# Kernel optimization log

Hardware: AMD Instinct MI355X
Metric: run time of the kernel (lower is better)

The kernel has to match this reference:

```python
import jax, jax.numpy as jnp
import numpy as np

B, NU, NT = 128, 32, 64          # batch, users/sample, antennas/sample
IN_F, H, OUT_F, NL = 128, 128, 16, 2
N_U, N_A = B * NU, B * NT        # total user / antenna nodes


def setup_inputs() -> dict:
    key = jax.random.key(0)
    ks = iter(jax.random.split(key, 40))
    p = lambda shape: jax.random.normal(next(ks), shape, jnp.float32) * 0.05
    inp = {
        'user_feat': jax.random.normal(next(ks), (N_U, IN_F), jnp.float32),
        'ant_noise': jax.random.normal(next(ks), (N_A, H), jnp.float32),
    }
    # complete bipartite edges within each batch sample
    b = np.arange(B)[:, None, None]
    u = np.arange(NU)[None, :, None]
    t = np.arange(NT)[None, None, :]
    su = np.broadcast_to(b * NU + u, (B, NU, NT)).reshape(-1)  # user global ids
    dt = np.broadcast_to(b * NT + t, (B, NU, NT)).reshape(-1)  # antenna global ids
    inp['src_u2a'] = jnp.asarray(su, jnp.int32)
    inp['dst_u2a'] = jnp.asarray(dt, jnp.int32)
    inp['src_a2u'] = jnp.asarray(dt, jnp.int32)
    inp['dst_a2u'] = jnp.asarray(su, jnp.int32)
    inp['W_ue'] = p((IN_F, H)); inp['b_ue'] = p((H,))
    inp['W_t'] = p((H, H));     inp['b_t'] = p((H,))
    for name in ['ca_aggr', 'ca_self', 'ca_comb', 'cu_aggr', 'cu_self', 'cu_comb']:
        inp[name + '_W'] = p((NL, H, H))
        inp[name + '_b'] = p((NL, H))
    inp['W_norm'] = p((H, OUT_F)); inp['b_norm'] = p((OUT_F,))
    return inp


def mlp(x, W, b):
    # stack of NL Linear(H,H) + ReLU, as in MLP module
    for i in range(W.shape[0]):
        x = jax.nn.relu(x @ W[i] + b[i])
    return x


def rel_conv(src_f, dst_f, src_idx, dst_idx, n_dst, aW, ab, sW, sb, cW, cb):
    # GraphConv2: mean-aggregate mlp_aggr(src) over in-edges, combine with mlp_self(dst)
    msg = mlp(src_f, aW, ab)                                   # [n_src, H]
    summed = jax.ops.segment_sum(msg[src_idx], dst_idx, num_segments=n_dst)
    deg = jax.ops.segment_sum(jnp.ones(dst_idx.shape, jnp.float32), dst_idx,
                              num_segments=n_dst)
    mean = summed / jnp.maximum(deg, 1.0)[:, None]
    return mlp(mlp(dst_f, sW, sb) + mean, cW, cb)


def reference(user_feat, ant_noise, src_u2a, dst_u2a, src_a2u, dst_a2u,
              W_ue, b_ue, W_t, b_t,
              ca_aggr_W, ca_aggr_b, ca_self_W, ca_self_b, ca_comb_W, ca_comb_b,
              cu_aggr_W, cu_aggr_b, cu_self_W, cu_self_b, cu_comb_W, cu_comb_b,
              W_norm, b_norm):
    # InitLayer
    hu = jax.nn.relu(user_feat @ W_ue + b_ue)                  # [B*NU, H]
    ant = jax.nn.relu(hu.reshape(B, NU, H).mean(axis=1) @ W_t + b_t)  # [B, H]
    ha = jnp.repeat(ant, NT, axis=0) + ant_noise               # [B*NT, H]
    # two applications of the SAME HeteroGraphConv (shared weights)
    for _ in range(2):
        na = rel_conv(hu, ha, src_u2a, dst_u2a, N_A,
                      ca_aggr_W, ca_aggr_b, ca_self_W, ca_self_b, ca_comb_W, ca_comb_b)
        nu = rel_conv(ha, hu, src_a2u, dst_a2u, N_U,
                      cu_aggr_W, cu_aggr_b, cu_self_W, cu_self_b, cu_comb_W, cu_comb_b)
        hu, ha = nu, na
    # NormLayer: project, split real/imag, normalize to unit modulus
    y = (ha @ W_norm + b_norm).reshape(B, NT, OUT_F)
    rf = OUT_F // 2
    re, im = y[..., :rf], y[..., rf:]
    mag = jnp.sqrt(re * re + im * im)
    return jnp.concatenate([re / mag, im / mag], axis=-1)      # [B, NT, OUT_F]
```

## Files before the change

### kernel.cpp

```cpp
#include <hip/hip_runtime.h>
#include <math.h>


using frag  = __attribute__((ext_vector_type(8))) short;
using f32x4 = __attribute__((ext_vector_type(4))) float;

#define LDST 136
#define SCOPE_AGT __HIP_MEMORY_SCOPE_AGENT

__device__ __forceinline__ float  bf2f(ushort u) { return __uint_as_float(((unsigned)u) << 16); }
__device__ __forceinline__ ushort f2bf(float f) {
    unsigned u = __float_as_uint(f);
    u += 0x7fff + ((u >> 16) & 1);
    return (ushort)(u >> 16);
}
__device__ __forceinline__ void gst4_sc(void* p, unsigned v) {
    asm volatile("global_store_dword %0, %1, off sc1" :: "v"(p), "v"(v) : "memory");
}

struct GP {
    const float *uf, *noise, *b_ue, *W_t, *b_t;
    const float *wsrc[13];
    const float *bias6[6];
    const float *Wn, *bn;
    float *out;
    ushort *WtAll;
    float *pE, *pA0, *pU0, *pA1;
    unsigned *cnt, *flg;
};

__device__ __forceinline__ void psync(unsigned* myf, unsigned* pf, unsigned s) {
    asm volatile("s_waitcnt vmcnt(0)" ::: "memory");
    __syncthreads();
    if (threadIdx.x == 0) {
        __hip_atomic_store(myf, s, __ATOMIC_RELAXED, SCOPE_AGT);
        while (__hip_atomic_load(pf, __ATOMIC_RELAXED, SCOPE_AGT) < s)
            __builtin_amdgcn_s_sleep(1);
    }
    __syncthreads();
}

template<int MT, bool MEANADD>
__device__ __forceinline__ void mlp_stage(const ushort* Xl, ushort* Yl,
    const ushort* __restrict__ Wt, const float* __restrict__ bias, const float* meanL)
{
    const int lane = threadIdx.x & 63, wave = threadIdx.x >> 6;
    const int q = lane >> 4, l15 = lane & 15;
    const int n0 = wave * 16;
    frag A[4];
#pragma unroll
    for (int kc = 0; kc < 4; ++kc)
        A[kc] = *(const frag*)(Wt + (n0 + l15) * 128 + kc * 32 + q * 8);
    const float4 bv = *(const float4*)(bias + n0 + q * 4);
    float4 mv = {0.f, 0.f, 0.f, 0.f};
    if (MEANADD) mv = *(const float4*)(meanL + n0 + q * 4);
#pragma unroll
    for (int mt = 0; mt < MT; ++mt) {
        frag Bv[4];
#pragma unroll
        for (int kc = 0; kc < 4; ++kc)
            Bv[kc] = *(const frag*)(Xl + (mt * 16 + l15) * LDST + kc * 32 + q * 8);
        f32x4 acc = {0.f, 0.f, 0.f, 0.f};
#pragma unroll
        for (int kc = 0; kc < 4; ++kc)
            acc = __builtin_amdgcn_mfma_f32_16x16x32_bf16(A[kc], Bv[kc], acc, 0, 0, 0);
        float v0 = acc[0] + bv.x, v1 = acc[1] + bv.y, v2 = acc[2] + bv.z, v3 = acc[3] + bv.w;
        v0 = v0 > 0.f ? v0 : 0.f; v1 = v1 > 0.f ? v1 : 0.f;
        v2 = v2 > 0.f ? v2 : 0.f; v3 = v3 > 0.f ? v3 : 0.f;
        if (MEANADD) { v0 += mv.x; v1 += mv.y; v2 += mv.z; v3 += mv.w; }
        ushort4 o = { f2bf(v0), f2bf(v1), f2bf(v2), f2bf(v3) };
        *(ushort4*)(Yl + (mt * 16 + l15) * LDST + n0 + q * 4) = o;
    }
}

template<int ROWS>
__device__ __forceinline__ void colsum(const ushort* buf, float* redL,
                                       float* ownDst, float* __restrict__ gDst)
{
    const int t = threadIdx.x, g = t >> 7, col = t & 127;
    float s = 0.f;
    for (int r = g; r < ROWS; r += 4) s += bf2f(buf[r * LDST + col]);
    redL[g * 128 + col] = s;
    __syncthreads();
    if (t < 128) {
        float tot = redL[t] + redL[128 + t] + redL[256 + t] + redL[384 + t];
        ownDst[t] = tot;
        gst4_sc(gDst + t, __float_as_uint(tot));
    }
    __syncthreads();
}

__device__ __forceinline__ void wslab(ushort* dst, float* slab,
                                      const float* __restrict__ W, int kb)
{
    {
        const int c = threadIdx.x;
        const int kr = c >> 5, c4 = c & 31;
        const float4 v = *(const float4*)(W + (kb * 16 + kr) * 128 + c4 * 4);
        slab[kr * 129 + c4 * 4 + 0] = v.x; slab[kr * 129 + c4 * 4 + 1] = v.y;
        slab[kr * 129 + c4 * 4 + 2] = v.z; slab[kr * 129 + c4 * 4 + 3] = v.w;
    }
    __syncthreads();
    for (int c = threadIdx.x; c < 1024; c += 512) {
        const int n = c >> 3, k2 = c & 7;
        const unsigned d = (unsigned)f2bf(slab[(2 * k2) * 129 + n])
                         | ((unsigned)f2bf(slab[(2 * k2 + 1) * 129 + n]) << 16);
        gst4_sc(dst + n * 128 + kb * 16 + 2 * k2, d);
    }
    __syncthreads();
}

__global__ __launch_bounds__(512, 1) void k_gnn(GP P)
{
    __shared__ __align__(16) ushort HU [16 * LDST];
    __shared__ __align__(16) ushort HU2[16 * LDST];
    __shared__ __align__(16) ushort HA [32 * LDST];
    __shared__ __align__(16) ushort HA2[32 * LDST];
    __shared__ __align__(16) ushort T0 [32 * LDST];
    __shared__ __align__(16) ushort T1 [32 * LDST];
    __shared__ float meanP[128], meanQ[128], antL[128], redL[512];

    const int blk = blockIdx.x, tid = threadIdx.x;
    const int b = blk >> 1, half = blk & 1;
    unsigned* myf = P.flg + blk * 32;
    unsigned* prf = P.flg + (blk ^ 1) * 32;
    const int prt = blk ^ 1;
    const ushort* Wt = P.WtAll;
    const float* const* bb = P.bias6;

    if (blk < 104)
        wslab(P.WtAll + (blk >> 3) * 16384, (float*)T1, P.wsrc[blk >> 3], blk & 7);

    {
        const int c = tid;
        const int r = c >> 5, k4 = c & 31;
        const float4 v = *(const float4*)(P.uf + (size_t)(b * 32 + half * 16 + r) * 128 + k4 * 4);
        ushort4 o = { f2bf(v.x), f2bf(v.y), f2bf(v.z), f2bf(v.w) };
        *(ushort4*)(T0 + r * LDST + k4 * 4) = o;
    }
    for (int c = tid; c < 1024; c += 512) {
        const int r = c >> 5, k4 = c & 31;
        const float4 v = *(const float4*)(P.noise + (size_t)(b * 64 + half * 32 + r) * 128 + k4 * 4);
        ushort4 o = { f2bf(v.x), f2bf(v.y), f2bf(v.z), f2bf(v.w) };
        *(ushort4*)(HA + r * LDST + k4 * 4) = o;
    }

    asm volatile("s_waitcnt vmcnt(0)" ::: "memory");
    __syncthreads();
    if (tid == 0) {
        if (blk < 104) {
            unsigned old = __hip_atomic_fetch_add(P.cnt, 1u, __ATOMIC_RELAXED, SCOPE_AGT);
            if (old == 103u) __hip_atomic_store(P.cnt + 32, 1u, __ATOMIC_RELAXED, SCOPE_AGT);
        }
        while (__hip_atomic_load(P.cnt + 32, __ATOMIC_RELAXED, SCOPE_AGT) < 1u)
            __builtin_amdgcn_s_sleep(4);
    }
    __syncthreads();

    mlp_stage<1, false>(T0, HU, Wt + 12 * 16384, P.b_ue, nullptr);
    __syncthreads();
    colsum<16>(HU, redL, meanP, P.pE + blk * 128);
    mlp_stage<1, false>(HU, T0, Wt + 0 * 16384, bb[0], nullptr);
    __syncthreads();
    mlp_stage<1, false>(T0, T1, Wt + 1 * 16384, bb[0] + 128, nullptr);
    __syncthreads();
    colsum<16>(T1, redL, meanQ, P.pA0 + blk * 128);
    psync(myf, prf, 1u);

    if (tid < 128) meanP[tid] = (meanP[tid] + P.pE[prt * 128 + tid]) * (1.f / 32.f);
    __syncthreads();
    {
        const int g = tid >> 7, col = tid & 127;
        float s = 0.f;
#pragma unroll 4
        for (int k = g * 32; k < g * 32 + 32; ++k) s += meanP[k] * P.W_t[k * 128 + col];
        redL[g * 128 + col] = s;
    }
    __syncthreads();
    if (tid < 128) {
        float a = P.b_t[tid] + redL[tid] + redL[128 + tid] + redL[256 + tid] + redL[384 + tid];
        antL[tid] = a > 0.f ? a : 0.f;
    }
    __syncthreads();
    for (int c = tid; c < 1024; c += 512) {
        const int r = c >> 5, k4 = c & 31;
        ushort4 h = *(ushort4*)(HA + r * LDST + k4 * 4);
        ushort4 o = { f2bf(bf2f(h.x) + antL[k4 * 4 + 0]), f2bf(bf2f(h.y) + antL[k4 * 4 + 1]),
                      f2bf(bf2f(h.z) + antL[k4 * 4 + 2]), f2bf(bf2f(h.w) + antL[k4 * 4 + 3]) };
        *(ushort4*)(HA + r * LDST + k4 * 4) = o;
    }
    __syncthreads();

    mlp_stage<2, false>(HA, T0, Wt + 6 * 16384, bb[3], nullptr);
    __syncthreads();
    mlp_stage<2, false>(T0, T1, Wt + 7 * 16384, bb[3] + 128, nullptr);
    __syncthreads();
    colsum<32>(T1, redL, meanP, P.pU0 + blk * 128);
    mlp_stage<2, false>(HA, T0, Wt + 2 * 16384, bb[1], nullptr);
    __syncthreads();
    psync(myf, prf, 2u);

    if (tid < 128) {
        meanQ[tid] = (meanQ[tid] + P.pA0[prt * 128 + tid]) * (1.f / 32.f);
        meanP[tid] = (meanP[tid] + P.pU0[prt * 128 + tid]) * (1.f / 64.f);
    }
    __syncthreads();
    mlp_stage<2, true >(T0, T1, Wt + 3 * 16384, bb[1] + 128, meanQ);
    __syncthreads();
    mlp_stage<2, false>(T1, T0, Wt + 4 * 16384, bb[2], nullptr);
    __syncthreads();
    mlp_stage<2, false>(T0, HA2, Wt + 5 * 16384, bb[2] + 128, nullptr);
    __syncthreads();
    mlp_stage<1, false>(HU, T0, Wt + 8 * 16384, bb[4], nullptr);
    __syncthreads();
    mlp_stage<1, true >(T0, T1, Wt + 9 * 16384, bb[4] + 128, meanP);
    __syncthreads();
    mlp_stage<1, false>(T1, T0, Wt + 10 * 16384, bb[5], nullptr);
    __syncthreads();
    mlp_stage<1, false>(T0, HU2, Wt + 11 * 16384, bb[5] + 128, nullptr);
    __syncthreads();

    mlp_stage<1, false>(HU2, T0, Wt + 0 * 16384, bb[0], nullptr);
    __syncthreads();
    mlp_stage<1, false>(T0, T1, Wt + 1 * 16384, bb[0] + 128, nullptr);
    __syncthreads();
    colsum<16>(T1, redL, meanQ, P.pA1 + blk * 128);
    mlp_stage<2, false>(HA2, T0, Wt + 2 * 16384, bb[1], nullptr);
    __syncthreads();
    psync(myf, prf, 3u);

    if (tid < 128) meanQ[tid] = (meanQ[tid] + P.pA1[prt * 128 + tid]) * (1.f / 32.f);
    __syncthreads();
    mlp_stage<2, true >(T0, T1, Wt + 3 * 16384, bb[1] + 128, meanQ);
    __syncthreads();
    mlp_stage<2, false>(T1, T0, Wt + 4 * 16384, bb[2], nullptr);
    __syncthreads();
    mlp_stage<2, false>(T0, T1, Wt + 5 * 16384, bb[2] + 128, nullptr);
    __syncthreads();

    float* WnS = (float*)T0;
    {
        const int c = tid;
        *(float4*)(WnS + c * 4) = *(const float4*)(P.Wn + c * 4);
    }
    __syncthreads();
    {
        const int row = tid >> 4, j = tid & 15;
        float acc = P.bn[j];
        const ushort* h = T1 + row * LDST;
#pragma unroll 4
        for (int k = 0; k < 128; ++k) acc += bf2f(h[k]) * WnS[k * 16 + j];
        redL[row * 16 + j] = acc;
        __syncthreads();
        const float re = redL[row * 16 + (j & 7)], im = redL[row * 16 + (j & 7) + 8];
        const float mag = sqrtf(re * re + im * im);
        const int a = b * 64 + half * 32 + row;
        P.out[a * 16 + j] = acc / mag;
    }
}

extern "C" void kernel_launch(void* const* d_in, const int* in_sizes, int n_in,
                              void* d_out, int out_size, void* d_ws, size_t ws_size,
                              hipStream_t stream)
{
    GP P;
    P.uf    = (const float*)d_in[0];
    P.noise = (const float*)d_in[1];
    const float* W_ue = (const float*)d_in[6];
    P.b_ue  = (const float*)d_in[7];
    P.W_t   = (const float*)d_in[8];
    P.b_t   = (const float*)d_in[9];
    const float* caW[3] = {(const float*)d_in[10], (const float*)d_in[12], (const float*)d_in[14]};
    const float* cab[3] = {(const float*)d_in[11], (const float*)d_in[13], (const float*)d_in[15]};
    const float* cuW[3] = {(const float*)d_in[16], (const float*)d_in[18], (const float*)d_in[20]};
    const float* cub[3] = {(const float*)d_in[17], (const float*)d_in[19], (const float*)d_in[21]};
    P.Wn  = (const float*)d_in[22];
    P.bn  = (const float*)d_in[23];
    P.out = (float*)d_out;

    P.wsrc[0]  = caW[0]; P.wsrc[1]  = caW[0] + 16384;
    P.wsrc[2]  = caW[1]; P.wsrc[3]  = caW[1] + 16384;
    P.wsrc[4]  = caW[2]; P.wsrc[5]  = caW[2] + 16384;
    P.wsrc[6]  = cuW[0]; P.wsrc[7]  = cuW[0] + 16384;
    P.wsrc[8]  = cuW[1]; P.wsrc[9]  = cuW[1] + 16384;
    P.wsrc[10] = cuW[2]; P.wsrc[11] = cuW[2] + 16384;
    P.wsrc[12] = W_ue;
    P.bias6[0] = cab[0]; P.bias6[1] = cab[1]; P.bias6[2] = cab[2];
    P.bias6[3] = cub[0]; P.bias6[4] = cub[1]; P.bias6[5] = cub[2];

    char* w = (char*)d_ws;
    P.cnt   = (unsigned*)w;
    P.flg   = (unsigned*)(w + 1024);
    P.WtAll = (ushort*)(w + 1024 + 32768);
    P.pE    = (float*)(P.WtAll + 13 * 16384);
    P.pA0   = P.pE  + 256 * 128;
    P.pU0   = P.pA0 + 256 * 128;
    P.pA1   = P.pU0 + 256 * 128;

    hipMemsetAsync(w, 0, 1024 + 32768, stream);
    k_gnn<<<dim3(256), dim3(512), 0, stream>>>(P);
}
```

Baseline: 140.3 us.

## Use one 1024-thread block per sample, removing pair sync and partial exchange

Each batch sample now runs in a single 1024-thread workgroup instead of two 512-thread workgroups. This removes the inter-block flag handshakes and the global partial-sum buffers used to share column means. Weight fragments for the next MLP stage are prefetched into registers during the current stage, and the final unit-modulus normalization uses a lane shuffle instead of a shared-memory round trip. In exchange, the grid drops from 256 to 128 blocks, so fewer compute units are busy, and each thread has more register pressure from the double-buffered fragments.

```diff
diff --git a/kernel.cpp b/kernel.cpp
--- a/kernel.cpp
+++ b/kernel.cpp
@@ -25,37 +25,28 @@
     const float *Wn, *bn;
     float *out;
     ushort *WtAll;
-    float *pE, *pA0, *pU0, *pA1;
-    unsigned *cnt, *flg;
+    unsigned *cnt;
 };
 
-__device__ __forceinline__ void psync(unsigned* myf, unsigned* pf, unsigned s) {
-    asm volatile("s_waitcnt vmcnt(0)" ::: "memory");
-    __syncthreads();
-    if (threadIdx.x == 0) {
-        __hip_atomic_store(myf, s, __ATOMIC_RELAXED, SCOPE_AGT);
-        while (__hip_atomic_load(pf, __ATOMIC_RELAXED, SCOPE_AGT) < s)
-            __builtin_amdgcn_s_sleep(1);
-    }
-    __syncthreads();
+struct AF { frag f[4]; };
+__device__ __forceinline__ AF loadA(const ushort* __restrict__ Wt, int n0, int l15, int q) {
+    AF r;
+#pragma unroll
+    for (int kc = 0; kc < 4; ++kc)
+        r.f[kc] = *(const frag*)(Wt + (n0 + l15) * 128 + kc * 32 + q * 8);
+    return r;
 }
 
 template<int MT, bool MEANADD>
-__device__ __forceinline__ void mlp_stage(const ushort* Xl, ushort* Yl,
-    const ushort* __restrict__ Wt, const float* __restrict__ bias, const float* meanL)
-{
-    const int lane = threadIdx.x & 63, wave = threadIdx.x >> 6;
-    const int q = lane >> 4, l15 = lane & 15;
-    const int n0 = wave * 16;
-    frag A[4];
-#pragma unroll
-    for (int kc = 0; kc < 4; ++kc)
-        A[kc] = *(const frag*)(Wt + (n0 + l15) * 128 + kc * 32 + q * 8);
+__device__ __forceinline__ void mlp_stage(const AF& A, const ushort* Xl, ushort* Yl,
+    const float* __restrict__ bias, const float* meanL, int n0, int l15, int q, int mg)
+{
     const float4 bv = *(const float4*)(bias + n0 + q * 4);
     float4 mv = {0.f, 0.f, 0.f, 0.f};
     if (MEANADD) mv = *(const float4*)(meanL + n0 + q * 4);
 #pragma unroll
-    for (int mt = 0; mt < MT; ++mt) {
+    for (int i = 0; i < MT / 2; ++i) {
+        const int mt = mg * (MT / 2) + i;
         frag Bv[4];
 #pragma unroll
         for (int kc = 0; kc < 4; ++kc)
@@ -63,7 +54,7 @@
         f32x4 acc = {0.f, 0.f, 0.f, 0.f};
 #pragma unroll
         for (int kc = 0; kc < 4; ++kc)
-            acc = __builtin_amdgcn_mfma_f32_16x16x32_bf16(A[kc], Bv[kc], acc, 0, 0, 0);
+            acc = __builtin_amdgcn_mfma_f32_16x16x32_bf16(A.f[kc], Bv[kc], acc, 0, 0, 0);
         float v0 = acc[0] + bv.x, v1 = acc[1] + bv.y, v2 = acc[2] + bv.z, v3 = acc[3] + bv.w;
         v0 = v0 > 0.f ? v0 : 0.f; v1 = v1 > 0.f ? v1 : 0.f;
         v2 = v2 > 0.f ? v2 : 0.f; v3 = v3 > 0.f ? v3 : 0.f;
@@ -74,26 +65,24 @@
 }
 
 template<int ROWS>
-__device__ __forceinline__ void colsum(const ushort* buf, float* redL,
-                                       float* ownDst, float* __restrict__ gDst)
-{
-    const int t = threadIdx.x, g = t >> 7, col = t & 127;
-    float s = 0.f;
-    for (int r = g; r < ROWS; r += 4) s += bf2f(buf[r * LDST + col]);
-    redL[g * 128 + col] = s;
-    __syncthreads();
-    if (t < 128) {
-        float tot = redL[t] + redL[128 + t] + redL[256 + t] + redL[384 + t];
-        ownDst[t] = tot;
-        gst4_sc(gDst + t, __float_as_uint(tot));
-    }
+__device__ __forceinline__ void colmean(const ushort* buf, float* redL, float* dst, float scale) {
+    const int t = threadIdx.x;
+    if (t < 512) {
+        const int g4 = t >> 7, col = t & 127;
+        float s = 0.f;
+#pragma unroll
+        for (int r = g4; r < ROWS; r += 4) s += bf2f(buf[r * LDST + col]);
+        redL[g4 * 128 + col] = s;
+    }
+    __syncthreads();
+    if (t < 128) dst[t] = (redL[t] + redL[128 + t] + redL[256 + t] + redL[384 + t]) * scale;
     __syncthreads();
 }
 
 __device__ __forceinline__ void wslab(ushort* dst, float* slab,
                                       const float* __restrict__ W, int kb)
 {
-    {
+    if (threadIdx.x < 512) {
         const int c = threadIdx.x;
         const int kr = c >> 5, c4 = c & 31;
         const float4 v = *(const float4*)(W + (kb * 16 + kr) * 128 + c4 * 4);
@@ -101,7 +90,8 @@
         slab[kr * 129 + c4 * 4 + 2] = v.z; slab[kr * 129 + c4 * 4 + 3] = v.w;
     }
     __syncthreads();
-    for (int c = threadIdx.x; c < 1024; c += 512) {
+    {
+        const int c = threadIdx.x;
         const int n = c >> 3, k2 = c & 7;
         const unsigned d = (unsigned)f2bf(slab[(2 * k2) * 129 + n])
                          | ((unsigned)f2bf(slab[(2 * k2 + 1) * 129 + n]) << 16);
@@ -110,37 +100,34 @@
     __syncthreads();
 }
 
-__global__ __launch_bounds__(512, 1) void k_gnn(GP P)
-{
-    __shared__ __align__(16) ushort HU [16 * LDST];
-    __shared__ __align__(16) ushort HU2[16 * LDST];
-    __shared__ __align__(16) ushort HA [32 * LDST];
-    __shared__ __align__(16) ushort HA2[32 * LDST];
-    __shared__ __align__(16) ushort T0 [32 * LDST];
-    __shared__ __align__(16) ushort T1 [32 * LDST];
-    __shared__ float meanP[128], meanQ[128], antL[128], redL[512];
-
-    const int blk = blockIdx.x, tid = threadIdx.x;
-    const int b = blk >> 1, half = blk & 1;
-    unsigned* myf = P.flg + blk * 32;
-    unsigned* prf = P.flg + (blk ^ 1) * 32;
-    const int prt = blk ^ 1;
+__global__ __launch_bounds__(1024, 1) void k_gnn(GP P)
+{
+    __shared__ __align__(16) ushort HU[32 * LDST];
+    __shared__ __align__(16) ushort HA[64 * LDST];
+    __shared__ __align__(16) ushort T0[64 * LDST];
+    __shared__ __align__(16) ushort T1[64 * LDST];
+    __shared__ float redL[512], mA[128], mB[128];
+
+    const int b = blockIdx.x, tid = threadIdx.x;
+    const int lane = tid & 63, wave = tid >> 6;
+    const int q = lane >> 4, l15 = lane & 15;
+    const int n0 = (wave & 7) * 16, mg = wave >> 3;
     const ushort* Wt = P.WtAll;
     const float* const* bb = P.bias6;
 
-    if (blk < 104)
-        wslab(P.WtAll + (blk >> 3) * 16384, (float*)T1, P.wsrc[blk >> 3], blk & 7);
+    if (b < 104)
+        wslab(P.WtAll + (b >> 3) * 16384, (float*)T1, P.wsrc[b >> 3], b & 7);
 
     {
-        const int c = tid;
-        const int r = c >> 5, k4 = c & 31;
-        const float4 v = *(const float4*)(P.uf + (size_t)(b * 32 + half * 16 + r) * 128 + k4 * 4);
+        const int r = tid >> 5, k4 = tid & 31;
+        const float4 v = *(const float4*)(P.uf + (size_t)(b * 32 + r) * 128 + k4 * 4);
         ushort4 o = { f2bf(v.x), f2bf(v.y), f2bf(v.z), f2bf(v.w) };
         *(ushort4*)(T0 + r * LDST + k4 * 4) = o;
     }
-    for (int c = tid; c < 1024; c += 512) {
+#pragma unroll
+    for (int c = tid; c < 2048; c += 1024) {
         const int r = c >> 5, k4 = c & 31;
-        const float4 v = *(const float4*)(P.noise + (size_t)(b * 64 + half * 32 + r) * 128 + k4 * 4);
+        const float4 v = *(const float4*)(P.noise + (size_t)(b * 64 + r) * 128 + k4 * 4);
         ushort4 o = { f2bf(v.x), f2bf(v.y), f2bf(v.z), f2bf(v.w) };
         *(ushort4*)(HA + r * LDST + k4 * 4) = o;
     }
@@ -148,7 +135,7 @@
     asm volatile("s_waitcnt vmcnt(0)" ::: "memory");
     __syncthreads();
     if (tid == 0) {
-        if (blk < 104) {
+        if (b < 104) {
             unsigned old = __hip_atomic_fetch_add(P.cnt, 1u, __ATOMIC_RELAXED, SCOPE_AGT);
             if (old == 103u) __hip_atomic_store(P.cnt + 32, 1u, __ATOMIC_RELAXED, SCOPE_AGT);
         }
@@ -157,105 +144,110 @@
     }
     __syncthreads();
 
-    mlp_stage<1, false>(T0, HU, Wt + 12 * 16384, P.b_ue, nullptr);
-    __syncthreads();
-    colsum<16>(HU, redL, meanP, P.pE + blk * 128);
-    mlp_stage<1, false>(HU, T0, Wt + 0 * 16384, bb[0], nullptr);
-    __syncthreads();
-    mlp_stage<1, false>(T0, T1, Wt + 1 * 16384, bb[0] + 128, nullptr);
-    __syncthreads();
-    colsum<16>(T1, redL, meanQ, P.pA0 + blk * 128);
-    psync(myf, prf, 1u);
-
-    if (tid < 128) meanP[tid] = (meanP[tid] + P.pE[prt * 128 + tid]) * (1.f / 32.f);
-    __syncthreads();
-    {
-        const int g = tid >> 7, col = tid & 127;
+    AF A, An = loadA(Wt + 12 * 16384, n0, l15, q);
+
+    A = An; An = loadA(Wt + 0 * 16384, n0, l15, q);
+    mlp_stage<2, false>(A, T0, HU, P.b_ue, nullptr, n0, l15, q, mg);
+    __syncthreads();
+    colmean<32>(HU, redL, mA, 1.f / 32.f);
+    if (tid < 512) {
+        const int g4 = tid >> 7, col = tid & 127;
         float s = 0.f;
 #pragma unroll 4
-        for (int k = g * 32; k < g * 32 + 32; ++k) s += meanP[k] * P.W_t[k * 128 + col];
-        redL[g * 128 + col] = s;
+        for (int k = g4 * 32; k < g4 * 32 + 32; ++k) s += mA[k] * P.W_t[k * 128 + col];
+        redL[g4 * 128 + col] = s;
     }
     __syncthreads();
     if (tid < 128) {
         float a = P.b_t[tid] + redL[tid] + redL[128 + tid] + redL[256 + tid] + redL[384 + tid];
-        antL[tid] = a > 0.f ? a : 0.f;
-    }
-    __syncthreads();
-    for (int c = tid; c < 1024; c += 512) {
+        mB[tid] = a > 0.f ? a : 0.f;
+    }
+    __syncthreads();
+#pragma unroll
+    for (int c = tid; c < 2048; c += 1024) {
         const int r = c >> 5, k4 = c & 31;
         ushort4 h = *(ushort4*)(HA + r * LDST + k4 * 4);
-        ushort4 o = { f2bf(bf2f(h.x) + antL[k4 * 4 + 0]), f2bf(bf2f(h.y) + antL[k4 * 4 + 1]),
-                      f2bf(bf2f(h.z) + antL[k4 * 4 + 2]), f2bf(bf2f(h.w) + antL[k4 * 4 + 3]) };
+        ushort4 o = { f2bf(bf2f(h.x) + mB[k4 * 4 + 0]), f2bf(bf2f(h.y) + mB[k4 * 4 + 1]),
+                      f2bf(bf2f(h.z) + mB[k4 * 4 + 2]), f2bf(bf2f(h.w) + mB[k4 * 4 + 3]) };
         *(ushort4*)(HA + r * LDST + k4 * 4) = o;
     }
     __syncthreads();
 
-    mlp_stage<2, false>(HA, T0, Wt + 6 * 16384, bb[3], nullptr);
-    __syncthreads();
-    mlp_stage<2, false>(T0, T1, Wt + 7 * 16384, bb[3] + 128, nullptr);
-    __syncthreads();
-    colsum<32>(T1, redL, meanP, P.pU0 + blk * 128);
-    mlp_stage<2, false>(HA, T0, Wt + 2 * 16384, bb[1], nullptr);
-    __syncthreads();
-    psync(myf, prf, 2u);
-
-    if (tid < 128) {
-        meanQ[tid] = (meanQ[tid] + P.pA0[prt * 128 + tid]) * (1.f / 32.f);
-        meanP[tid] = (meanP[tid] + P.pU0[prt * 128 + tid]) * (1.f / 64.f);
-    }
-    __syncthreads();
-    mlp_stage<2, true >(T0, T1, Wt + 3 * 16384, bb[1] + 128, meanQ);
-    __syncthreads();
-    mlp_stage<2, false>(T1, T0, Wt + 4 * 16384, bb[2], nullptr);
-    __syncthreads();
-    mlp_stage<2, false>(T0, HA2, Wt + 5 * 16384, bb[2] + 128, nullptr);
-    __syncthreads();
-    mlp_stage<1, false>(HU, T0, Wt + 8 * 16384, bb[4], nullptr);
-    __syncthreads();
-    mlp_stage<1, true >(T0, T1, Wt + 9 * 16384, bb[4] + 128, meanP);
-    __syncthreads();
-    mlp_stage<1, false>(T1, T0, Wt + 10 * 16384, bb[5], nullptr);
-    __syncthreads();
-    mlp_stage<1, false>(T0, HU2, Wt + 11 * 16384, bb[5] + 128, nullptr);
-    __syncthreads();
-
-    mlp_stage<1, false>(HU2, T0, Wt + 0 * 16384, bb[0], nullptr);
-    __syncthreads();
-    mlp_stage<1, false>(T0, T1, Wt + 1 * 16384, bb[0] + 128, nullptr);
-    __syncthreads();
-    colsum<16>(T1, redL, meanQ, P.pA1 + blk * 128);
-    mlp_stage<2, false>(HA2, T0, Wt + 2 * 16384, bb[1], nullptr);
-    __syncthreads();
-    psync(myf, prf, 3u);
-
-    if (tid < 128) meanQ[tid] = (meanQ[tid] + P.pA1[prt * 128 + tid]) * (1.f / 32.f);
-    __syncthreads();
-    mlp_stage<2, true >(T0, T1, Wt + 3 * 16384, bb[1] + 128, meanQ);
-    __syncthreads();
-    mlp_stage<2, false>(T1, T0, Wt + 4 * 16384, bb[2], nullptr);
-    __syncthreads();
-    mlp_stage<2, false>(T0, T1, Wt + 5 * 16384, bb[2] + 128, nullptr);
+    A = An; An = loadA(Wt + 1 * 16384, n0, l15, q);
+    mlp_stage<2, false>(A, HU, T0, bb[0], nullptr, n0, l15, q, mg);
+    __syncthreads();
+    A = An; An = loadA(Wt + 6 * 16384, n0, l15, q);
+    mlp_stage<2, false>(A, T0, T1, bb[0] + 128, nullptr, n0, l15, q, mg);
+    __syncthreads();
+    colmean<32>(T1, redL, mA, 1.f / 32.f);
+
+    A = An; An = loadA(Wt + 7 * 16384, n0, l15, q);
+    mlp_stage<4, false>(A, HA, T0, bb[3], nullptr, n0, l15, q, mg);
+    __syncthreads();
+    A = An; An = loadA(Wt + 2 * 16384, n0, l15, q);
+    mlp_stage<4, false>(A, T0, T1, bb[3] + 128, nullptr, n0, l15, q, mg);
+    __syncthreads();
+    colmean<64>(T1, redL, mB, 1.f / 64.f);
+
+    A = An; An = loadA(Wt + 3 * 16384, n0, l15, q);
+    mlp_stage<4, false>(A, HA, T0, bb[1], nullptr, n0, l15, q, mg);
+    __syncthreads();
+    A = An; An = loadA(Wt + 4 * 16384, n0, l15, q);
+    mlp_stage<4, true >(A, T0, T1, bb[1] + 128, mA, n0, l15, q, mg);
+    __syncthreads();
+    A = An; An = loadA(Wt + 5 * 16384, n0, l15, q);
+    mlp_stage<4, false>(A, T1, T0, bb[2], nullptr, n0, l15, q, mg);
+    __syncthreads();
+    A = An; An = loadA(Wt + 8 * 16384, n0, l15, q);
+    mlp_stage<4, false>(A, T0, HA, bb[2] + 128, nullptr, n0, l15, q, mg);
+    __syncthreads();
+
+    A = An; An = loadA(Wt + 9 * 16384, n0, l15, q);
+    mlp_stage<2, false>(A, HU, T0, bb[4], nullptr, n0, l15, q, mg);
+    __syncthreads();
+    A = An; An = loadA(Wt + 10 * 16384, n0, l15, q);
+    mlp_stage<2, true >(A, T0, T1, bb[4] + 128, mB, n0, l15, q, mg);
+    __syncthreads();
+    A = An; An = loadA(Wt + 11 * 16384, n0, l15, q);
+    mlp_stage<2, false>(A, T1, T0, bb[5], nullptr, n0, l15, q, mg);
+    __syncthreads();
+    A = An; An = loadA(Wt + 0 * 16384, n0, l15, q);
+    mlp_stage<2, false>(A, T0, HU, bb[5] + 128, nullptr, n0, l15, q, mg);
+    __syncthreads();
+
+    A = An; An = loadA(Wt + 1 * 16384, n0, l15, q);
+    mlp_stage<2, false>(A, HU, T0, bb[0], nullptr, n0, l15, q, mg);
+    __syncthreads();
+    A = An; An = loadA(Wt + 2 * 16384, n0, l15, q);
+    mlp_stage<2, false>(A, T0, T1, bb[0] + 128, nullptr, n0, l15, q, mg);
+    __syncthreads();
+    colmean<32>(T1, redL, mA, 1.f / 32.f);
+
+    A = An; An = loadA(Wt + 3 * 16384, n0, l15, q);
+    mlp_stage<4, false>(A, HA, T0, bb[1], nullptr, n0, l15, q, mg);
+    __syncthreads();
+    A = An; An = loadA(Wt + 4 * 16384, n0, l15, q);
+    mlp_stage<4, true >(A, T0, T1, bb[1] + 128, mA, n0, l15, q, mg);
+    __syncthreads();
+    A = An; An = loadA(Wt + 5 * 16384, n0, l15, q);
+    mlp_stage<4, false>(A, T1, T0, bb[2], nullptr, n0, l15, q, mg);
+    __syncthreads();
+    A = An;
+    mlp_stage<4, false>(A, T0, T1, bb[2] + 128, nullptr, n0, l15, q, mg);
     __syncthreads();
 
     float* WnS = (float*)T0;
-    {
-        const int c = tid;
-        *(float4*)(WnS + c * 4) = *(const float4*)(P.Wn + c * 4);
-    }
+    if (tid < 512) *(float4*)(WnS + tid * 4) = *(const float4*)(P.Wn + tid * 4);
     __syncthreads();
     {
         const int row = tid >> 4, j = tid & 15;
         float acc = P.bn[j];
         const ushort* h = T1 + row * LDST;
-#pragma unroll 4
+#pragma unroll 8
         for (int k = 0; k < 128; ++k) acc += bf2f(h[k]) * WnS[k * 16 + j];
-        redL[row * 16 + j] = acc;
-        __syncthreads();
-        const float re = redL[row * 16 + (j & 7)], im = redL[row * 16 + (j & 7) + 8];
-        const float mag = sqrtf(re * re + im * im);
-        const int a = b * 64 + half * 32 + row;
-        P.out[a * 16 + j] = acc / mag;
+        const float other = __shfl_xor(acc, 8);
+        const float mag = sqrtf(acc * acc + other * other);
+        P.out[(size_t)(b * 64 + row) * 16 + j] = acc / mag;
     }
 }
 
@@ -290,13 +282,8 @@
 
     char* w = (char*)d_ws;
     P.cnt   = (unsigned*)w;
-    P.flg   = (unsigned*)(w + 1024);
-    P.WtAll = (ushort*)(w + 1024 + 32768);
-    P.pE    = (float*)(P.WtAll + 13 * 16384);
-    P.pA0   = P.pE  + 256 * 128;
-    P.pU0   = P.pA0 + 256 * 128;
-    P.pA1   = P.pU0 + 256 * 128;
-
-    hipMemsetAsync(w, 0, 1024 + 32768, stream);
-    k_gnn<<<dim3(256), dim3(512), 0, stream>>>(P);
-}
+    P.WtAll = (ushort*)(w + 1024);
+
+    hipMemsetAsync(w, 0, 1024, stream);
+    k_gnn<<<dim3(128), dim3(1024), 0, stream>>>(P);
+}
```

New measurement: 149.2 us. +6.4%, slower.

## Drop global weight-transpose phase; prefetch fp32 weights per stage into registers

Applied to the files above, without the earlier changes.

Removes the initial phase where 104 blocks converted weights to a transposed bf16 workspace, along with the grid-wide barrier that made every block wait for it. Each wave now loads its fp32 weight slice straight from global memory, converts it to bf16 fragments in registers, and prefetches the next stage's weights while the current MFMA stage runs. Biases are staged once in LDS, one mean update is moved earlier, and the final normalisation uses a lane shuffle in place of an LDS round trip. The trade is that every block repeats strided, uncoalesced fp32 weight reads and conversion work, and the prefetch buffer adds about 32 registers per thread.

```diff
diff --git a/kernel.cpp b/kernel.cpp
--- a/kernel.cpp
+++ b/kernel.cpp
@@ -20,13 +20,12 @@
 
 struct GP {
     const float *uf, *noise, *b_ue, *W_t, *b_t;
-    const float *wsrc[13];
+    const float *Wm[13];
     const float *bias6[6];
     const float *Wn, *bn;
     float *out;
-    ushort *WtAll;
     float *pE, *pA0, *pU0, *pA1;
-    unsigned *cnt, *flg;
+    unsigned *flg;
 };
 
 __device__ __forceinline__ void psync(unsigned* myf, unsigned* pf, unsigned s) {
@@ -40,18 +39,35 @@
     __syncthreads();
 }
 
+struct PF { float v[32]; };
+struct AF { frag f[4]; };
+__device__ __forceinline__ PF prefA(const float* __restrict__ W, int n0, int l15, int q) {
+    PF p;
+    const float* base = W + (size_t)(q * 8) * 128 + n0 + l15;
+#pragma unroll
+    for (int kc = 0; kc < 4; ++kc)
+#pragma unroll
+        for (int j = 0; j < 8; ++j)
+            p.v[kc * 8 + j] = base[(kc * 32 + j) * 128];
+    return p;
+}
+__device__ __forceinline__ AF convA(const PF& p) {
+    AF a;
+#pragma unroll
+    for (int kc = 0; kc < 4; ++kc) {
+        frag f;
+#pragma unroll
+        for (int j = 0; j < 8; ++j) f[j] = (short)f2bf(p.v[kc * 8 + j]);
+        a.f[kc] = f;
+    }
+    return a;
+}
+
 template<int MT, bool MEANADD>
-__device__ __forceinline__ void mlp_stage(const ushort* Xl, ushort* Yl,
-    const ushort* __restrict__ Wt, const float* __restrict__ bias, const float* meanL)
+__device__ __forceinline__ void mlp_stage(const AF& A, const ushort* Xl, ushort* Yl,
+    const float* biasL, const float* meanL, int n0, int l15, int q)
 {
-    const int lane = threadIdx.x & 63, wave = threadIdx.x >> 6;
-    const int q = lane >> 4, l15 = lane & 15;
-    const int n0 = wave * 16;
-    frag A[4];
-#pragma unroll
-    for (int kc = 0; kc < 4; ++kc)
-        A[kc] = *(const frag*)(Wt + (n0 + l15) * 128 + kc * 32 + q * 8);
-    const float4 bv = *(const float4*)(bias + n0 + q * 4);
+    const float4 bv = *(const float4*)(biasL + n0 + q * 4);
     float4 mv = {0.f, 0.f, 0.f, 0.f};
     if (MEANADD) mv = *(const float4*)(meanL + n0 + q * 4);
 #pragma unroll
@@ -63,7 +79,7 @@
         f32x4 acc = {0.f, 0.f, 0.f, 0.f};
 #pragma unroll
         for (int kc = 0; kc < 4; ++kc)
-            acc = __builtin_amdgcn_mfma_f32_16x16x32_bf16(A[kc], Bv[kc], acc, 0, 0, 0);
+            acc = __builtin_amdgcn_mfma_f32_16x16x32_bf16(A.f[kc], Bv[kc], acc, 0, 0, 0);
         float v0 = acc[0] + bv.x, v1 = acc[1] + bv.y, v2 = acc[2] + bv.z, v3 = acc[3] + bv.w;
         v0 = v0 > 0.f ? v0 : 0.f; v1 = v1 > 0.f ? v1 : 0.f;
         v2 = v2 > 0.f ? v2 : 0.f; v3 = v3 > 0.f ? v3 : 0.f;
@@ -79,6 +95,7 @@
 {
     const int t = threadIdx.x, g = t >> 7, col = t & 127;
     float s = 0.f;
+#pragma unroll
     for (int r = g; r < ROWS; r += 4) s += bf2f(buf[r * LDST + col]);
     redL[g * 128 + col] = s;
     __syncthreads();
@@ -90,84 +107,64 @@
     __syncthreads();
 }
 
-__device__ __forceinline__ void wslab(ushort* dst, float* slab,
-                                      const float* __restrict__ W, int kb)
-{
-    {
-        const int c = threadIdx.x;
-        const int kr = c >> 5, c4 = c & 31;
-        const float4 v = *(const float4*)(W + (kb * 16 + kr) * 128 + c4 * 4);
-        slab[kr * 129 + c4 * 4 + 0] = v.x; slab[kr * 129 + c4 * 4 + 1] = v.y;
-        slab[kr * 129 + c4 * 4 + 2] = v.z; slab[kr * 129 + c4 * 4 + 3] = v.w;
-    }
-    __syncthreads();
-    for (int c = threadIdx.x; c < 1024; c += 512) {
-        const int n = c >> 3, k2 = c & 7;
-        const unsigned d = (unsigned)f2bf(slab[(2 * k2) * 129 + n])
-                         | ((unsigned)f2bf(slab[(2 * k2 + 1) * 129 + n]) << 16);
-        gst4_sc(dst + n * 128 + kb * 16 + 2 * k2, d);
-    }
-    __syncthreads();
-}
-
 __global__ __launch_bounds__(512, 1) void k_gnn(GP P)
 {
-    __shared__ __align__(16) ushort HU [16 * LDST];
-    __shared__ __align__(16) ushort HU2[16 * LDST];
-    __shared__ __align__(16) ushort HA [32 * LDST];
-    __shared__ __align__(16) ushort HA2[32 * LDST];
-    __shared__ __align__(16) ushort T0 [32 * LDST];
-    __shared__ __align__(16) ushort T1 [32 * LDST];
-    __shared__ float meanP[128], meanQ[128], antL[128], redL[512];
+    __shared__ __align__(16) ushort HU[16 * LDST];
+    __shared__ __align__(16) ushort HA[32 * LDST];
+    __shared__ __align__(16) ushort T0[32 * LDST];
+    __shared__ __align__(16) ushort T1[32 * LDST];
+    __shared__ __align__(16) float  biasL[1792];
+    __shared__ __align__(16) float  redL[512];
+    __shared__ __align__(16) float  meanP[128], meanQ[128], antL[128];
 
     const int blk = blockIdx.x, tid = threadIdx.x;
-    const int b = blk >> 1, half = blk & 1;
+    const int b = blk >> 1, half = blk & 1, prt = blk ^ 1;
+    const int lane = tid & 63, wave = tid >> 6;
+    const int q = lane >> 4, l15 = lane & 15;
+    const int n0 = wave * 16;
     unsigned* myf = P.flg + blk * 32;
-    unsigned* prf = P.flg + (blk ^ 1) * 32;
-    const int prt = blk ^ 1;
-    const ushort* Wt = P.WtAll;
-    const float* const* bb = P.bias6;
-
-    if (blk < 104)
-        wslab(P.WtAll + (blk >> 3) * 16384, (float*)T1, P.wsrc[blk >> 3], blk & 7);
+    unsigned* prf = P.flg + prt * 32;
+
+    PF p = prefA(P.Wm[12], n0, l15, q);
 
     {
-        const int c = tid;
-        const int r = c >> 5, k4 = c & 31;
+        const int r = tid >> 5, k4 = tid & 31;
         const float4 v = *(const float4*)(P.uf + (size_t)(b * 32 + half * 16 + r) * 128 + k4 * 4);
         ushort4 o = { f2bf(v.x), f2bf(v.y), f2bf(v.z), f2bf(v.w) };
         *(ushort4*)(T0 + r * LDST + k4 * 4) = o;
     }
+#pragma unroll
     for (int c = tid; c < 1024; c += 512) {
         const int r = c >> 5, k4 = c & 31;
         const float4 v = *(const float4*)(P.noise + (size_t)(b * 64 + half * 32 + r) * 128 + k4 * 4);
         ushort4 o = { f2bf(v.x), f2bf(v.y), f2bf(v.z), f2bf(v.w) };
         *(ushort4*)(HA + r * LDST + k4 * 4) = o;
     }
-
-    asm volatile("s_waitcnt vmcnt(0)" ::: "memory");
-    __syncthreads();
-    if (tid == 0) {
-        if (blk < 104) {
-            unsigned old = __hip_atomic_fetch_add(P.cnt, 1u, __ATOMIC_RELAXED, SCOPE_AGT);
-            if (old == 103u) __hip_atomic_store(P.cnt + 32, 1u, __ATOMIC_RELAXED, SCOPE_AGT);
-        }
-        while (__hip_atomic_load(P.cnt + 32, __ATOMIC_RELAXED, SCOPE_AGT) < 1u)
-            __builtin_amdgcn_s_sleep(4);
-    }
-    __syncthreads();
-
-    mlp_stage<1, false>(T0, HU, Wt + 12 * 16384, P.b_ue, nullptr);
+    if (tid < 128) biasL[tid] = P.b_ue[tid];
+    if (tid < 128) biasL[1664 + tid] = P.b_t[tid];
+#pragma unroll
+    for (int r = 0; r < 6; ++r)
+        if (tid < 256) biasL[128 + r * 256 + tid] = P.bias6[r][tid];
+    __syncthreads();
+
+    AF A;
+    A = convA(p); p = prefA(P.Wm[0], n0, l15, q);
+    mlp_stage<1, false>(A, T0, HU, biasL + 0, nullptr, n0, l15, q);
     __syncthreads();
     colsum<16>(HU, redL, meanP, P.pE + blk * 128);
-    mlp_stage<1, false>(HU, T0, Wt + 0 * 16384, bb[0], nullptr);
-    __syncthreads();
-    mlp_stage<1, false>(T0, T1, Wt + 1 * 16384, bb[0] + 128, nullptr);
+    A = convA(p); p = prefA(P.Wm[1], n0, l15, q);
+    mlp_stage<1, false>(A, HU, T0, biasL + 128, nullptr, n0, l15, q);
+    __syncthreads();
+    A = convA(p); p = prefA(P.Wm[6], n0, l15, q);
+    mlp_stage<1, false>(A, T0, T1, biasL + 256, nullptr, n0, l15, q);
     __syncthreads();
     colsum<16>(T1, redL, meanQ, P.pA0 + blk * 128);
     psync(myf, prf, 1u);
 
-    if (tid < 128) meanP[tid] = (meanP[tid] + P.pE[prt * 128 + tid]) * (1.f / 32.f);
+    if (tid < 128) {
+        meanP[tid] = (meanP[tid] + P.pE[prt * 128 + tid]) * (1.f / 32.f);
+        meanQ[tid] = (meanQ[tid] + P.pA0[prt * 128 + tid]) * (1.f / 32.f);
+    }
     __syncthreads();
     {
         const int g = tid >> 7, col = tid & 127;
@@ -178,10 +175,11 @@
     }
     __syncthreads();
     if (tid < 128) {
-        float a = P.b_t[tid] + redL[tid] + redL[128 + tid] + redL[256 + tid] + redL[384 + tid];
+        float a = biasL[1664 + tid] + redL[tid] + redL[128 + tid] + redL[256 + tid] + redL[384 + tid];
         antL[tid] = a > 0.f ? a : 0.f;
     }
     __syncthreads();
+#pragma unroll
     for (int c = tid; c < 1024; c += 512) {
         const int r = c >> 5, k4 = c & 31;
         ushort4 h = *(ushort4*)(HA + r * LDST + k4 * 4);
@@ -191,71 +189,78 @@
     }
     __syncthreads();
 
-    mlp_stage<2, false>(HA, T0, Wt + 6 * 16384, bb[3], nullptr);
-    __syncthreads();
-    mlp_stage<2, false>(T0, T1, Wt + 7 * 16384, bb[3] + 128, nullptr);
+    A = convA(p); p = prefA(P.Wm[7], n0, l15, q);
+    mlp_stage<2, false>(A, HA, T0, biasL + 896, nullptr, n0, l15, q);
+    __syncthreads();
+    A = convA(p); p = prefA(P.Wm[2], n0, l15, q);
+    mlp_stage<2, false>(A, T0, T1, biasL + 1024, nullptr, n0, l15, q);
     __syncthreads();
     colsum<32>(T1, redL, meanP, P.pU0 + blk * 128);
-    mlp_stage<2, false>(HA, T0, Wt + 2 * 16384, bb[1], nullptr);
+    A = convA(p); p = prefA(P.Wm[3], n0, l15, q);
+    mlp_stage<2, false>(A, HA, T0, biasL + 384, nullptr, n0, l15, q);
     __syncthreads();
     psync(myf, prf, 2u);
-
-    if (tid < 128) {
-        meanQ[tid] = (meanQ[tid] + P.pA0[prt * 128 + tid]) * (1.f / 32.f);
+    if (tid < 128)
         meanP[tid] = (meanP[tid] + P.pU0[prt * 128 + tid]) * (1.f / 64.f);
-    }
-    __syncthreads();
-    mlp_stage<2, true >(T0, T1, Wt + 3 * 16384, bb[1] + 128, meanQ);
-    __syncthreads();
-    mlp_stage<2, false>(T1, T0, Wt + 4 * 16384, bb[2], nullptr);
-    __syncthreads();
-    mlp_stage<2, false>(T0, HA2, Wt + 5 * 16384, bb[2] + 128, nullptr);
-    __syncthreads();
-    mlp_stage<1, false>(HU, T0, Wt + 8 * 16384, bb[4], nullptr);
-    __syncthreads();
-    mlp_stage<1, true >(T0, T1, Wt + 9 * 16384, bb[4] + 128, meanP);
-    __syncthreads();
-    mlp_stage<1, false>(T1, T0, Wt + 10 * 16384, bb[5], nullptr);
-    __syncthreads();
-    mlp_stage<1, false>(T0, HU2, Wt + 11 * 16384, bb[5] + 128, nullptr);
-    __syncthreads();
-
-    mlp_stage<1, false>(HU2, T0, Wt + 0 * 16384, bb[0], nullptr);
-    __syncthreads();
-    mlp_stage<1, false>(T0, T1, Wt + 1 * 16384, bb[0] + 128, nullptr);
+    __syncthreads();
+    A = convA(p); p = prefA(P.Wm[4], n0, l15, q);
+    mlp_stage<2, true >(A, T0, T1, biasL + 512, meanQ, n0, l15, q);
+    __syncthreads();
+    A = convA(p); p = prefA(P.Wm[5], n0, l15, q);
+    mlp_stage<2, false>(A, T1, T0, biasL + 640, nullptr, n0, l15, q);
+    __syncthreads();
+    A = convA(p); p = prefA(P.Wm[8], n0, l15, q);
+    mlp_stage<2, false>(A, T0, HA, biasL + 768, nullptr, n0, l15, q);
+    __syncthreads();
+    A = convA(p); p = prefA(P.Wm[9], n0, l15, q);
+    mlp_stage<1, false>(A, HU, T0, biasL + 1152, nullptr, n0, l15, q);
+    __syncthreads();
+    A = convA(p); p = prefA(P.Wm[10], n0, l15, q);
+    mlp_stage<1, true >(A, T0, T1, biasL + 1280, meanP, n0, l15, q);
+    __syncthreads();
+    A = convA(p); p = prefA(P.Wm[11], n0, l15, q);
+    mlp_stage<1, false>(A, T1, T0, biasL + 1408, nullptr, n0, l15, q);
+    __syncthreads();
+    A = convA(p); p = prefA(P.Wm[0], n0, l15, q);
+    mlp_stage<1, false>(A, T0, HU, biasL + 1536, nullptr, n0, l15, q);
+    __syncthreads();
+
+    A = convA(p); p = prefA(P.Wm[1], n0, l15, q);
+    mlp_stage<1, false>(A, HU, T0, biasL + 128, nullptr, n0, l15, q);
+    __syncthreads();
+    A = convA(p); p = prefA(P.Wm[2], n0, l15, q);
+    mlp_stage<1, false>(A, T0, T1, biasL + 256, nullptr, n0, l15, q);
     __syncthreads();
     colsum<16>(T1, redL, meanQ, P.pA1 + blk * 128);
-    mlp_stage<2, false>(HA2, T0, Wt + 2 * 16384, bb[1], nullptr);
+    A = convA(p); p = prefA(P.Wm[3], n0, l15, q);
+    mlp_stage<2, false>(A, HA, T0, biasL + 384, nullptr, n0, l15, q);
     __syncthreads();
     psync(myf, prf, 3u);
-
-    if (tid < 128) meanQ[tid] = (meanQ[tid] + P.pA1[prt * 128 + tid]) * (1.f / 32.f);
-    __syncthreads();
-    mlp_stage<2, true >(T0, T1, Wt + 3 * 16384, bb[1] + 128, meanQ);
-    __syncthreads();
-    mlp_stage<2, false>(T1, T0, Wt + 4 * 16384, bb[2], nullptr);
-    __syncthreads();
-    mlp_stage<2, false>(T0, T1, Wt + 5 * 16384, bb[2] + 128, nullptr);
+    if (tid < 128)
+        meanQ[tid] = (meanQ[tid] + P.pA1[prt * 128 + tid]) * (1.f / 32.f);
+    __syncthreads();
+    A = convA(p); p = prefA(P.Wm[4], n0, l15, q);
+    mlp_stage<2, true >(A, T0, T1, biasL + 512, meanQ, n0, l15, q);
+    __syncthreads();
+    A = convA(p); p = prefA(P.Wm[5], n0, l15, q);
+    mlp_stage<2, false>(A, T1, T0, biasL + 640, nullptr, n0, l15, q);
+    __syncthreads();
+    A = convA(p);
+    mlp_stage<2, false>(A, T0, T1, biasL + 768, nullptr, n0, l15, q);
     __syncthreads();
 
     float* WnS = (float*)T0;
-    {
-        const int c = tid;
-        *(float4*)(WnS + c * 4) = *(const float4*)(P.Wn + c * 4);
-    }
+    *(float4*)(WnS + tid * 4) = *(const float4*)(P.Wn + tid * 4);
     __syncthreads();
     {
         const int row = tid >> 4, j = tid & 15;
         float acc = P.bn[j];
         const ushort* h = T1 + row * LDST;
-#pragma unroll 4
+#pragma unroll 8
         for (int k = 0; k < 128; ++k) acc += bf2f(h[k]) * WnS[k * 16 + j];
-        redL[row * 16 + j] = acc;
-        __syncthreads();
-        const float re = redL[row * 16 + (j & 7)], im = redL[row * 16 + (j & 7) + 8];
-        const float mag = sqrtf(re * re + im * im);
-        const int a = b * 64 + half * 32 + row;
-        P.out[a * 16 + j] = acc / mag;
+        const float other = __shfl_xor(acc, 8);
+        const float mag = sqrtf(acc * acc + other * other);
+        P.out[(size_t)(b * 64 + half * 32 + row) * 16 + j] = acc / mag;
     }
 }
 
@@ -278,25 +283,23 @@
     P.bn  = (const float*)d_in[23];
     P.out = (float*)d_out;
 
-    P.wsrc[0]  = caW[0]; P.wsrc[1]  = caW[0] + 16384;
-    P.wsrc[2]  = caW[1]; P.wsrc[3]  = caW[1] + 16384;
-    P.wsrc[4]  = caW[2]; P.wsrc[5]  = caW[2] + 16384;
-    P.wsrc[6]  = cuW[0]; P.wsrc[7]  = cuW[0] + 16384;
-    P.wsrc[8]  = cuW[1]; P.wsrc[9]  = cuW[1] + 16384;
-    P.wsrc[10] = cuW[2]; P.wsrc[11] = cuW[2] + 16384;
-    P.wsrc[12] = W_ue;
+    P.Wm[0]  = caW[0]; P.Wm[1]  = caW[0] + 16384;
+    P.Wm[2]  = caW[1]; P.Wm[3]  = caW[1] + 16384;
+    P.Wm[4]  = caW[2]; P.Wm[5]  = caW[2] + 16384;
+    P.Wm[6]  = cuW[0]; P.Wm[7]  = cuW[0] + 16384;
+    P.Wm[8]  = cuW[1]; P.Wm[9]  = cuW[1] + 16384;
+    P.Wm[10] = cuW[2]; P.Wm[11] = cuW[2] + 16384;
+    P.Wm[12] = W_ue;
     P.bias6[0] = cab[0]; P.bias6[1] = cab[1]; P.bias6[2] = cab[2];
     P.bias6[3] = cub[0]; P.bias6[4] = cub[1]; P.bias6[5] = cub[2];
 
     char* w = (char*)d_ws;
-    P.cnt   = (unsigned*)w;
-    P.flg   = (unsigned*)(w + 1024);
-    P.WtAll = (ushort*)(w + 1024 + 32768);
-    P.pE    = (float*)(P.WtAll + 13 * 16384);
-    P.pA0   = P.pE  + 256 * 128;
-    P.pU0   = P.pA0 + 256 * 128;
-    P.pA1   = P.pU0 + 256 * 128;
-
-    hipMemsetAsync(w, 0, 1024 + 32768, stream);
+    P.flg = (unsigned*)w;
+    P.pE  = (float*)(w + 32768);
+    P.pA0 = P.pE  + 256 * 128;
+    P.pU0 = P.pA0 + 256 * 128;
+    P.pA1 = P.pU0 + 256 * 128;
+
+    hipMemsetAsync(w, 0, 32768, stream);
     k_gnn<<<dim3(256), dim3(512), 0, stream>>>(P);
 }
```

Result: faster. 132.3 us (-5.7%).
